# Kernel optimization log

Measured on AMD Instinct MI355X. Metric: run time of the kernel, lower is better.

## Reference

```python
import jax, jax.numpy as jnp
import numpy as np

DIM = 1024
D_STATE = 16
D_CONV = 4
EXPAND = 2
D_INNER = EXPAND * DIM          # 2048
DT_RANK = (DIM + 15) // 16      # 64 (math.ceil(d_model/16))
BSZ = 2
SEQ = 2048


def setup_inputs() -> dict:
    key = jax.random.key(0)
    ks = jax.random.split(key, 8)
    g = lambda k, shape, scale: (jax.random.normal(k, shape, jnp.float32) * scale)
    return {
        "x": g(ks[0], (BSZ, SEQ, DIM), 1.0),
        # in_proj: Linear(d_model -> 2*d_inner, bias=False)
        "W_in": g(ks[1], (2 * D_INNER, DIM), DIM ** -0.5),
        # depthwise causal conv1d: groups=d_inner, kernel d_conv, bias=True
        "conv_w": g(ks[2], (D_INNER, 1, D_CONV), D_CONV ** -0.5),
        "conv_b": jnp.zeros((D_INNER,), jnp.float32),
        # x_proj: Linear(d_inner -> dt_rank + 2*d_state, bias=False)
        "W_xproj": g(ks[3], (DT_RANK + 2 * D_STATE, D_INNER), D_INNER ** -0.5),
        # dt_proj: Linear(dt_rank -> d_inner, bias=True)
        "W_dt": g(ks[4], (D_INNER, DT_RANK), DT_RANK ** -0.5),
        "b_dt": g(ks[5], (D_INNER,), 0.1),
        # S4D-real init: A = -exp(A_log), A_log = log(1..d_state)
        "A_log": jnp.log(jnp.broadcast_to(
            jnp.arange(1, D_STATE + 1, dtype=jnp.float32), (D_INNER, D_STATE))),
        "D": jnp.ones((D_INNER,), jnp.float32),
        # out_proj: Linear(d_inner -> d_model, bias=False)
        "W_out": g(ks[6], (DIM, D_INNER), D_INNER ** -0.5),
        # wrapper LayerNorm(dim)
        "gamma": jnp.ones((DIM,), jnp.float32),
        "beta": jnp.zeros((DIM,), jnp.float32),
    }


def reference(x, W_in, conv_w, conv_b, W_xproj, W_dt, b_dt,
              A_log, D, W_out, gamma, beta):
    B, L, _ = x.shape
    # ---- input projection, split into conv path and gate ----
    xz = x @ W_in.T                              # (B, L, 2*d_inner)
    xc, z = jnp.split(xz, 2, axis=-1)
    # ---- depthwise causal conv1d + SiLU ----
    xt = jnp.transpose(xc, (0, 2, 1))            # (B, d_inner, L)
    conv = jax.lax.conv_general_dilated(
        xt, conv_w, window_strides=(1,), padding=[(D_CONV - 1, 0)],
        dimension_numbers=("NCH", "OIH", "NCH"), feature_group_count=D_INNER)
    u = jax.nn.silu(jnp.transpose(conv + conv_b[None, :, None], (0, 2, 1)))  # (B,L,d_inner)
    # ---- input-dependent delta, B, C ----
    xdbc = u @ W_xproj.T                          # (B, L, dt_rank + 2*d_state)
    dt = xdbc[..., :DT_RANK]
    Bm = xdbc[..., DT_RANK:DT_RANK + D_STATE]     # (B, L, d_state)
    Cm = xdbc[..., DT_RANK + D_STATE:]            # (B, L, d_state)
    delta = jax.nn.softplus(dt @ W_dt.T + b_dt)   # (B, L, d_inner)
    A = -jnp.exp(A_log)                           # (d_inner, d_state)
    # ---- selective scan: h_t = exp(dt*A) h_{t-1} + dt*B_t*u_t ; y_t = <h_t, C_t> ----
    def step(h, inputs):
        d_t, u_t, B_t, C_t = inputs               # (B,d_inner),(B,d_inner),(B,S),(B,S)
        dA = jnp.exp(d_t[:, :, None] * A)         # (B, d_inner, S)
        h = h * dA + (d_t * u_t)[:, :, None] * B_t[:, None, :]
        y = jnp.einsum("bds,bs->bd", h, C_t)
        return h, y
    tm = lambda a: jnp.transpose(a, (1, 0, 2))    # time-major for scan
    h0 = jnp.zeros((B, D_INNER, D_STATE), x.dtype)
    _, ys = jax.lax.scan(step, h0, (tm(delta), tm(u), tm(Bm), tm(Cm)))
    y = jnp.transpose(ys, (1, 0, 2)) + u * D      # skip term D*u
    y = y * jax.nn.silu(z)                        # gate
    out = y @ W_out.T                             # (B, L, dim)
    # ---- wrapper LayerNorm(dim), eps=1e-5 ----
    mean = out.mean(-1, keepdims=True)
    var = out.var(-1, keepdims=True)
    return (out - mean) * jax.lax.rsqrt(var + 1e-5) * gamma + beta
```

## Files before the change

### kernel.cpp

```cpp
#include <hip/hip_runtime.h>
#include <stdint.h>

typedef unsigned short u16;
typedef __bf16 bf16x8 __attribute__((ext_vector_type(8)));
typedef unsigned short u16x8 __attribute__((ext_vector_type(8)));
typedef unsigned short u16x4 __attribute__((ext_vector_type(4)));
typedef float f32x4 __attribute__((ext_vector_type(4)));

#define BSZ 2
#define SEQ 2048
#define DIM 1024
#define D_INNER 2048
#define DT_RANK 64
#define D_STATE 16
#define XPROJ_N 96
#define NCHUNK 32
#define CHUNK_T 64
#define LOG2E 1.44269504f

#define N_X   4194304
#define N_W   4194304
#define N_WX  196608
#define N_WDT 131072
#define N_WO  2097152
#define N_XD  393216

__device__ __forceinline__ float bf2f(u16 h) {
    return __uint_as_float(((unsigned)h) << 16);
}
__device__ __forceinline__ u16 f2bf(float f) {
    unsigned u = __float_as_uint(f);
    unsigned r = (u + 0x7FFFu + ((u >> 16) & 1u)) >> 16;
    return (u16)r;
}

__device__ __forceinline__ f32x4 mfma16(bf16x8 a, bf16x8 b, f32x4 c) {
    return __builtin_amdgcn_mfma_f32_16x16x32_bf16(a, b, c, 0, 0, 0);
}

__device__ __forceinline__ void gload_lds16(const void* g, void* l) {
    __builtin_amdgcn_global_load_lds(
        (const __attribute__((address_space(1))) unsigned int*)(uintptr_t)g,
        (__attribute__((address_space(3))) unsigned int*)(uintptr_t)l,
        16, 0, 0);
}

__device__ __forceinline__ void split4(const float* __restrict__ in,
                                       u16* __restrict__ hi, u16* __restrict__ lo,
                                       long i)
{
    f32x4 v = *(const f32x4*)(in + i);
    u16x4 h, l;
    #pragma unroll
    for (int j = 0; j < 4; j++) {
        u16 hh = f2bf(v[j]);
        h[j] = hh;
        l[j] = f2bf(v[j] - bf2f(hh));
    }
    *(u16x4*)(hi + i) = h;
    *(u16x4*)(lo + i) = l;
}

__global__ __launch_bounds__(256)
void megasplit4(const float* __restrict__ x,  u16* __restrict__ xh,  u16* __restrict__ xl,
                const float* __restrict__ w,  u16* __restrict__ wh,  u16* __restrict__ wl,
                const float* __restrict__ wx, u16* __restrict__ wxh, u16* __restrict__ wxl,
                const float* __restrict__ wd, u16* __restrict__ wdh, u16* __restrict__ wdl)
{
    long i = ((long)blockIdx.x * 256 + threadIdx.x) * 4;
    if (i < N_X) { split4(x, xh, xl, i); return; }
    i -= N_X;
    if (i < N_W) { split4(w, wh, wl, i); return; }
    i -= N_W;
    if (i < N_WX) { split4(wx, wxh, wxl, i); return; }
    i -= N_WX;
    if (i < N_WDT) { split4(wd, wdh, wdl, i); }
}

#define PH_TOP                                                                \
    __builtin_amdgcn_sched_barrier(0);                                        \
    __builtin_amdgcn_s_barrier();                                             \
    asm volatile("s_waitcnt lgkmcnt(0)" ::: "memory");                        \
    __builtin_amdgcn_sched_barrier(0);                                        \
    __builtin_amdgcn_s_setprio(1);
#define PH_BOT                                                                \
    __builtin_amdgcn_s_setprio(0);                                            \
    __builtin_amdgcn_sched_barrier(0);                                        \
    __builtin_amdgcn_s_barrier();

__global__ __launch_bounds__(512, 2)
void gemm256_xz(const u16* __restrict__ xh, const u16* __restrict__ xl,
                const u16* __restrict__ wh, const u16* __restrict__ wl,
                u16* __restrict__ xc, float* __restrict__ z)
{
    __shared__ u16 lds[65536];

    const int tid  = threadIdx.x;
    const int w    = tid >> 6;
    const int lane = tid & 63;
    const int r16  = lane & 15;
    const int quad = lane >> 4;
    const int wr   = w >> 2;
    const int wc   = w & 3;
    const long m0  = (long)blockIdx.y * 256;
    const long n0  = (long)blockIdx.x * 256;

    const int c0 = tid, c1 = tid + 512;
    const int ma0 = c0 >> 2, kc0 = ((c0 & 3) ^ ((ma0 >> 1) & 3)) * 8;
    const int ma1 = c1 >> 2, kc1 = ((c1 & 3) ^ ((ma1 >> 1) & 3)) * 8;
    const int arow0 = ((int)m0 + ma0) * DIM + kc0;
    const int arow1 = ((int)m0 + ma1) * DIM + kc1;
    const int brow0 = ((int)n0 + ma0) * DIM + kc0;
    const int brow1 = ((int)n0 + ma1) * DIM + kc1;

    int caof[8], cbof[4];
    #pragma unroll
    for (int i = 0; i < 8; i++) {
        int m = wr * 128 + i * 16 + r16;
        caof[i] = (m * 4 + (quad ^ ((m >> 1) & 3))) * 8;
    }
    #pragma unroll
    for (int j = 0; j < 4; j++) {
        int n = wc * 64 + j * 16 + r16;
        cbof[j] = (n * 4 + (quad ^ ((n >> 1) & 3))) * 8;
    }

    f32x4 acc[8][4];
    #pragma unroll
    for (int i = 0; i < 8; i++)
        #pragma unroll
        for (int j = 0; j < 4; j++) acc[i][j] = {0.f, 0.f, 0.f, 0.f};

    gload_lds16(xh + arow0, lds + c0 * 8);
    gload_lds16(xh + arow1, lds + c1 * 8);
    gload_lds16(xl + arow0, lds + 8192 + c0 * 8);
    gload_lds16(xl + arow1, lds + 8192 + c1 * 8);
    gload_lds16(wh + brow0, lds + 16384 + c0 * 8);
    gload_lds16(wh + brow1, lds + 16384 + c1 * 8);
    gload_lds16(wl + brow0, lds + 24576 + c0 * 8);
    gload_lds16(wl + brow1, lds + 24576 + c1 * 8);
    asm volatile("s_waitcnt vmcnt(0)" ::: "memory");
    __builtin_amdgcn_s_barrier();

    int kt = 0;
#define XZ_FTILE(CUR, SN)                                                     \
  {                                                                           \
    int st = kt + 1; if (st > 31) st = 31;                                    \
    const int kb = st * 32;                                                   \
    const u16* AHp = lds + (CUR) * 32768;                                     \
    const u16* ALp = AHp + 8192;                                              \
    const u16* BHp = AHp + 16384;                                             \
    const u16* BLp = AHp + 24576;                                             \
    u16* Sb = lds + (SN) * 32768;                                             \
    bf16x8 a0[4], a1[4], fbh[4], fbl[4];                                      \
                            \
    _Pragma("unroll") for (int j = 0; j < 4; j++)                             \
        fbh[j] = *(const bf16x8*)(BHp + cbof[j]);                             \
    _Pragma("unroll") for (int i = 0; i < 4; i++)                             \
        a0[i] = *(const bf16x8*)(AHp + caof[i]);                              \
    gload_lds16(xh + arow0 + kb, Sb + c0 * 8);                                \
    gload_lds16(xh + arow1 + kb, Sb + c1 * 8);                                \
    PH_TOP                                                                    \
    _Pragma("unroll") for (int i = 0; i < 4; i++)                             \
      _Pragma("unroll") for (int j = 0; j < 4; j++)                           \
        acc[i][j] = mfma16(a0[i], fbh[j], acc[i][j]);                         \
    PH_BOT                                                                    \
                                \
    _Pragma("unroll") for (int i = 0; i < 4; i++)                             \
        a1[i] = *(const bf16x8*)(AHp + caof[4 + i]);                          \
    gload_lds16(xl + arow0 + kb, Sb + 8192 + c0 * 8);                         \
    gload_lds16(xl + arow1 + kb, Sb + 8192 + c1 * 8);                         \
    PH_TOP                                                                    \
    _Pragma("unroll") for (int i = 0; i < 4; i++)                             \
      _Pragma("unroll") for (int j = 0; j < 4; j++)                           \
        acc[4 + i][j] = mfma16(a1[i], fbh[j], acc[4 + i][j]);                 \
    PH_BOT                                                                    \
                        \
    _Pragma("unroll") for (int j = 0; j < 4; j++)                             \
        fbl[j] = *(const bf16x8*)(BLp + cbof[j]);                             \
    gload_lds16(wh + brow0 + kb, Sb + 16384 + c0 * 8);                        \
    gload_lds16(wh + brow1 + kb, Sb + 16384 + c1 * 8);                        \
    PH_TOP                                                                    \
    _Pragma("unroll") for (int i = 0; i < 4; i++)                             \
      _Pragma("unroll") for (int j = 0; j < 4; j++)                           \
        acc[i][j] = mfma16(a0[i], fbl[j], acc[i][j]);                         \
    PH_BOT                                                                    \
                             \
    gload_lds16(wl + brow0 + kb, Sb + 24576 + c0 * 8);                        \
    gload_lds16(wl + brow1 + kb, Sb + 24576 + c1 * 8);                        \
    PH_TOP                                                                    \
    _Pragma("unroll") for (int i = 0; i < 4; i++)                             \
      _Pragma("unroll") for (int j = 0; j < 4; j++)                           \
        acc[4 + i][j] = mfma16(a1[i], fbl[j], acc[4 + i][j]);                 \
    PH_BOT                                                                    \
                   \
    _Pragma("unroll") for (int i = 0; i < 4; i++)                             \
        a0[i] = *(const bf16x8*)(ALp + caof[i]);                              \
    PH_TOP                                                                    \
    _Pragma("unroll") for (int i = 0; i < 4; i++)                             \
      _Pragma("unroll") for (int j = 0; j < 4; j++)                           \
        acc[i][j] = mfma16(a0[i], fbh[j], acc[i][j]);                         \
    PH_BOT                                                                    \
                      \
    _Pragma("unroll") for (int i = 0; i < 4; i++)                             \
        a1[i] = *(const bf16x8*)(ALp + caof[4 + i]);                          \
    PH_TOP                                                                    \
    _Pragma("unroll") for (int i = 0; i < 4; i++)                             \
      _Pragma("unroll") for (int j = 0; j < 4; j++)                           \
        acc[4 + i][j] = mfma16(a1[i], fbh[j], acc[4 + i][j]);                 \
    __builtin_amdgcn_s_setprio(0);                                            \
    __builtin_amdgcn_sched_barrier(0);                                        \
    asm volatile("s_waitcnt vmcnt(0)" ::: "memory");                          \
    __builtin_amdgcn_s_barrier();                                             \
    kt++;                                                                     \
  }

    #pragma unroll 1
    for (int it = 0; it < 16; it++) {
        XZ_FTILE(0, 1)
        XZ_FTILE(1, 0)
    }
#undef XZ_FTILE

    asm volatile("s_waitcnt vmcnt(0)" ::: "memory");

    const bool isz = (n0 >= 2048);
    #pragma unroll
    for (int i = 0; i < 8; i++) {
        #pragma unroll
        for (int j = 0; j < 4; j++) {
            long col = n0 + wc * 64 + j * 16 + r16;
            #pragma unroll
            for (int r = 0; r < 4; r++) {
                long row = m0 + wr * 128 + i * 16 + quad * 4 + r;
                if (!isz) xc[row * (long)D_INNER + col] = f2bf(acc[i][j][r]);
                else      z[row * (long)D_INNER + (col - D_INNER)] = acc[i][j][r];
            }
        }
    }
}

__global__ __launch_bounds__(512, 2)
void gemm256_out(const u16* __restrict__ A, const u16* __restrict__ Bh,
                 const u16* __restrict__ Bl, float* __restrict__ OutBase)
{
    __shared__ u16 lds[40960];

    const int tid  = threadIdx.x;
    const int w    = tid >> 6;
    const int lane = tid & 63;
    const int r16  = lane & 15;
    const int quad = lane >> 4;
    const int wr   = w >> 2;
    const int wc   = w & 3;
    const long m0  = (long)blockIdx.y * 128;
    const long n0  = (long)blockIdx.x * 256;
    const int  kz  = blockIdx.z;
    const int  kbase = kz * 1024;
    float* Out = OutBase + (long)kz * 4194304;

    const int maA = tid >> 2, kcA = ((tid & 3) ^ ((maA >> 1) & 3)) * 8;
    const int arow = ((int)m0 + maA) * D_INNER + kbase + kcA;
    const int c0 = tid, c1 = tid + 512;
    const int mb0 = c0 >> 2, kb0 = ((c0 & 3) ^ ((mb0 >> 1) & 3)) * 8;
    const int mb1 = c1 >> 2, kb1 = ((c1 & 3) ^ ((mb1 >> 1) & 3)) * 8;
    const int brow0 = ((int)n0 + mb0) * D_INNER + kbase + kb0;
    const int brow1 = ((int)n0 + mb1) * D_INNER + kbase + kb1;

    int caof[4], cbof[4];
    #pragma unroll
    for (int i = 0; i < 4; i++) {
        int m = wr * 64 + i * 16 + r16;
        caof[i] = (m * 4 + (quad ^ ((m >> 1) & 3))) * 8;
    }
    #pragma unroll
    for (int j = 0; j < 4; j++) {
        int n = wc * 64 + j * 16 + r16;
        cbof[j] = (n * 4 + (quad ^ ((n >> 1) & 3))) * 8;
    }

    f32x4 acc[4][4];
    #pragma unroll
    for (int i = 0; i < 4; i++)
        #pragma unroll
        for (int j = 0; j < 4; j++) acc[i][j] = {0.f, 0.f, 0.f, 0.f};

    gload_lds16(A  + arow,  lds + tid * 8);
    gload_lds16(Bh + brow0, lds + 4096 + c0 * 8);
    gload_lds16(Bh + brow1, lds + 4096 + c1 * 8);
    gload_lds16(Bl + brow0, lds + 12288 + c0 * 8);
    gload_lds16(Bl + brow1, lds + 12288 + c1 * 8);
    asm volatile("s_waitcnt vmcnt(0)" ::: "memory");
    __builtin_amdgcn_s_barrier();

    int kt = 0;
#define O2_TILE(CUR, SN)                                                      \
  {                                                                           \
    int st = kt + 1; if (st > 31) st = 31;                                    \
    const int kb = st * 32;                                                   \
    const u16* Ap  = lds + (CUR) * 20480;                                     \
    const u16* BHp = Ap + 4096;                                               \
    const u16* BLp = Ap + 12288;                                              \
    u16* Sb = lds + (SN) * 20480;                                             \
    bf16x8 fa[4], fb[4];                                                      \
                            \
    _Pragma("unroll") for (int j = 0; j < 4; j++)                             \
        fb[j] = *(const bf16x8*)(BHp + cbof[j]);                              \
    _Pragma("unroll") for (int i = 0; i < 4; i++)                             \
        fa[i] = *(const bf16x8*)(Ap + caof[i]);                               \
    gload_lds16(A + arow + kb, Sb + tid * 8);                                 \
    PH_TOP                                                                    \
    _Pragma("unroll") for (int i = 0; i < 4; i++)                             \
      _Pragma("unroll") for (int j = 0; j < 4; j++)                           \
        acc[i][j] = mfma16(fa[i], fb[j], acc[i][j]);                          \
    PH_BOT                                                                    \
                 \
    _Pragma("unroll") for (int j = 0; j < 4; j++)                             \
        fb[j] = *(const bf16x8*)(BLp + cbof[j]);                              \
    gload_lds16(Bh + brow0 + kb, Sb + 4096 + c0 * 8);                         \
    gload_lds16(Bh + brow1 + kb, Sb + 4096 + c1 * 8);                         \
    gload_lds16(Bl + brow0 + kb, Sb + 12288 + c0 * 8);                        \
    gload_lds16(Bl + brow1 + kb, Sb + 12288 + c1 * 8);                        \
    PH_TOP                                                                    \
    _Pragma("unroll") for (int i = 0; i < 4; i++)                             \
      _Pragma("unroll") for (int j = 0; j < 4; j++)                           \
        acc[i][j] = mfma16(fa[i], fb[j], acc[i][j]);                          \
    __builtin_amdgcn_s_setprio(0);                                            \
    __builtin_amdgcn_sched_barrier(0);                                        \
    asm volatile("s_waitcnt vmcnt(0)" ::: "memory");                          \
    __builtin_amdgcn_s_barrier();                                             \
    kt++;                                                                     \
  }

    #pragma unroll 1
    for (int it = 0; it < 16; it++) {
        O2_TILE(0, 1)
        O2_TILE(1, 0)
    }
#undef O2_TILE

    asm volatile("s_waitcnt vmcnt(0)" ::: "memory");

    #pragma unroll
    for (int i = 0; i < 4; i++) {
        #pragma unroll
        for (int j = 0; j < 4; j++) {
            long col = n0 + wc * 64 + j * 16 + r16;
            #pragma unroll
            for (int r = 0; r < 4; r++) {
                long row = m0 + wr * 64 + i * 16 + quad * 4 + r;
                Out[row * (long)DIM + col] = acc[i][j][r];
            }
        }
    }
}

__global__ __launch_bounds__(64)
void gemm_dt32(const u16* __restrict__ Ah, const u16* __restrict__ Al, int lda,
               const u16* __restrict__ Bh, const u16* __restrict__ Bl, int ldb,
               float* __restrict__ C, int ldc, const float* __restrict__ bias)
{
    const int lane = threadIdx.x;
    const int r16  = lane & 15;
    const int quad = lane >> 4;
    const long m0 = (long)blockIdx.y * 32;
    const long n0 = (long)blockIdx.x * 32;

    const u16* Ah0 = Ah + (m0 + r16) * (long)lda + quad * 8;
    const u16* Ah1 = Ah0 + 16L * lda;
    const u16* Al0 = Al + (m0 + r16) * (long)lda + quad * 8;
    const u16* Al1 = Al0 + 16L * lda;
    const u16* Bh0 = Bh + (n0 + r16) * (long)ldb + quad * 8;
    const u16* Bh1 = Bh0 + 16L * ldb;
    const u16* Bl0 = Bl + (n0 + r16) * (long)ldb + quad * 8;
    const u16* Bl1 = Bl0 + 16L * ldb;

    f32x4 acc00 = {0,0,0,0}, acc01 = {0,0,0,0}, acc10 = {0,0,0,0}, acc11 = {0,0,0,0};

    #pragma unroll
    for (int k = 0; k < DT_RANK; k += 32) {
        bf16x8 a0h = *(const bf16x8*)(Ah0 + k);
        bf16x8 a1h = *(const bf16x8*)(Ah1 + k);
        bf16x8 a0l = *(const bf16x8*)(Al0 + k);
        bf16x8 a1l = *(const bf16x8*)(Al1 + k);
        bf16x8 b0h = *(const bf16x8*)(Bh0 + k);
        bf16x8 b1h = *(const bf16x8*)(Bh1 + k);
        bf16x8 b0l = *(const bf16x8*)(Bl0 + k);
        bf16x8 b1l = *(const bf16x8*)(Bl1 + k);
        acc00 = mfma16(a0h, b0h, acc00); acc00 = mfma16(a0h, b0l, acc00); acc00 = mfma16(a0l, b0h, acc00);
        acc01 = mfma16(a0h, b1h, acc01); acc01 = mfma16(a0h, b1l, acc01); acc01 = mfma16(a0l, b1h, acc01);
        acc10 = mfma16(a1h, b0h, acc10); acc10 = mfma16(a1h, b0l, acc10); acc10 = mfma16(a1l, b0h, acc10);
        acc11 = mfma16(a1h, b1h, acc11); acc11 = mfma16(a1h, b1l, acc11); acc11 = mfma16(a1l, b1h, acc11);
    }

    #pragma unroll
    for (int i = 0; i < 2; i++) {
        #pragma unroll
        for (int j = 0; j < 2; j++) {
            f32x4 v = (i == 0) ? (j == 0 ? acc00 : acc01) : (j == 0 ? acc10 : acc11);
            long col = n0 + j * 16 + r16;
            #pragma unroll
            for (int r = 0; r < 4; r++) {
                long row = m0 + i * 16 + quad * 4 + r;
                float x = v[r] + bias[col];
                x = (x > 15.f) ? x : log1pf(__expf(x));
                C[row * (long)ldc + col] = x;
            }
        }
    }
}

__global__ __launch_bounds__(64)
void gemm3_skp(const u16* __restrict__ A, int lda,
               const u16* __restrict__ Bh, const u16* __restrict__ Bl, int ldb,
               float* __restrict__ Cpart, int ldc, int K0)
{
    const int lane = threadIdx.x;
    const int r16  = lane & 15;
    const int quad = lane >> 4;
    const long m0 = (long)blockIdx.y * 32;
    const long n0 = (long)blockIdx.x * 32;
    const int kbase = blockIdx.z * K0;
    float* C = Cpart + (long)blockIdx.z * N_XD;

    const u16* Ap0 = A  + (m0 + r16) * (long)lda + quad * 8 + kbase;
    const u16* Ap1 = Ap0 + 16L * lda;
    const u16* Bh0 = Bh + (n0 + r16) * (long)ldb + quad * 8 + kbase;
    const u16* Bh1 = Bh0 + 16L * ldb;
    const u16* Bl0 = Bl + (n0 + r16) * (long)ldb + quad * 8 + kbase;
    const u16* Bl1 = Bl0 + 16L * ldb;

    f32x4 acc00 = {0,0,0,0}, acc01 = {0,0,0,0}, acc10 = {0,0,0,0}, acc11 = {0,0,0,0};

    for (int k = 0; k < K0; k += 32) {
        bf16x8 a0 = *(const bf16x8*)(Ap0 + k);
        bf16x8 a1 = *(const bf16x8*)(Ap1 + k);
        bf16x8 b0h = *(const bf16x8*)(Bh0 + k);
        bf16x8 b1h = *(const bf16x8*)(Bh1 + k);
        bf16x8 b0l = *(const bf16x8*)(Bl0 + k);
        bf16x8 b1l = *(const bf16x8*)(Bl1 + k);
        acc00 = mfma16(a0, b0h, acc00); acc00 = mfma16(a0, b0l, acc00);
        acc01 = mfma16(a0, b1h, acc01); acc01 = mfma16(a0, b1l, acc01);
        acc10 = mfma16(a1, b0h, acc10); acc10 = mfma16(a1, b0l, acc10);
        acc11 = mfma16(a1, b1h, acc11); acc11 = mfma16(a1, b1l, acc11);
    }

    #pragma unroll
    for (int i = 0; i < 2; i++) {
        #pragma unroll
        for (int j = 0; j < 2; j++) {
            f32x4 v = (i == 0) ? (j == 0 ? acc00 : acc01) : (j == 0 ? acc10 : acc11);
            long col = n0 + j * 16 + r16;
            #pragma unroll
            for (int r = 0; r < 4; r++) {
                long row = m0 + i * 16 + quad * 4 + r;
                C[row * (long)ldc + col] = v[r];
            }
        }
    }
}

__global__ __launch_bounds__(256)
void combine3(const float* __restrict__ part, float* __restrict__ xdbc,
              u16* __restrict__ hi, u16* __restrict__ lo)
{
    long i = ((long)blockIdx.x * 256 + threadIdx.x) * 4;
    if (i >= N_XD) return;
    f32x4 s = *(const f32x4*)(part + i);
    #pragma unroll
    for (int j = 1; j < 8; j++) {
        f32x4 p = *(const f32x4*)(part + (long)j * N_XD + i);
        s[0] += p[0]; s[1] += p[1]; s[2] += p[2]; s[3] += p[3];
    }
    *(f32x4*)(xdbc + i) = s;
    u16x4 h, l;
    #pragma unroll
    for (int j = 0; j < 4; j++) {
        u16 hh = f2bf(s[j]);
        h[j] = hh;
        l[j] = f2bf(s[j] - bf2f(hh));
    }
    *(u16x4*)(hi + i) = h;
    *(u16x4*)(lo + i) = l;
}

__global__ __launch_bounds__(256)
void conv_silu(const u16* __restrict__ xc, const float* __restrict__ cw,
               const float* __restrict__ cb, u16* __restrict__ u)
{
    long idx = ((long)blockIdx.x * 256 + threadIdx.x) * 8;
    int t  = (int)((idx >> 11) & 2047);
    int d0 = (int)(idx & 2047);

    bf16x8 xrow[4];
    #pragma unroll
    for (int j = 0; j < 4; j++) {
        int tt = t - 3 + j;
        if (tt >= 0) xrow[j] = *(const bf16x8*)(xc + idx + (long)(j - 3) * D_INNER);
        else         xrow[j] = bf16x8{0,0,0,0,0,0,0,0};
    }
    u16x8 out;
    #pragma unroll
    for (int e = 0; e < 8; e++) {
        int d = d0 + e;
        float acc = cb[d];
        #pragma unroll
        for (int j = 0; j < 4; j++)
            acc += cw[d * 4 + j] * (float)xrow[j][e];
        out[e] = f2bf(acc / (1.f + __expf(-acc)));
    }
    *(u16x8*)(u + idx) = out;
}

__global__ __launch_bounds__(256)
void scan_partA(const float* __restrict__ delta, const u16* __restrict__ u,
                const float* __restrict__ xdbc, const float* __restrict__ A_log,
                float* __restrict__ hbuf, float* __restrict__ sdelta,
                const float* __restrict__ wout, u16* __restrict__ wouth,
                u16* __restrict__ woutl)
{
    const int d = blockIdx.x * 256 + threadIdx.x;
    const int c = blockIdx.y;
    const int b = blockIdx.z;
    const int t0 = c * CHUNK_T;

    float Af[16];
    #pragma unroll
    for (int s = 0; s < 16; s++) Af[s] = -__expf(A_log[d * 16 + s]) * LOG2E;
    bool fast = true;
    #pragma unroll
    for (int s = 0; s < 16; s++)
        fast = fast && (fabsf(Af[s] - (float)(s + 1) * Af[0]) < 1e-3f * (float)(s + 1));

    float h[16];
    #pragma unroll
    for (int s = 0; s < 16; s++) h[s] = 0.f;
    float sd = 0.f;

    const float* dptr = delta + ((long)b * SEQ + t0) * D_INNER + d;
    const u16*   uptr = u     + ((long)b * SEQ + t0) * D_INNER + d;
    const float* xp   = xdbc  + ((long)b * SEQ + t0) * XPROJ_N;

    if (fast) {
        const float Af0 = Af[0];
        for (int t = 0; t < CHUNK_T; t++) {
            float dl = dptr[(long)t * D_INNER];
            float uu = bf2f(uptr[(long)t * D_INNER]);
            f32x4 B0 = *(const f32x4*)(xp + t * XPROJ_N + DT_RANK);
            f32x4 B1 = *(const f32x4*)(xp + t * XPROJ_N + DT_RANK + 4);
            f32x4 B2 = *(const f32x4*)(xp + t * XPROJ_N + DT_RANK + 8);
            f32x4 B3 = *(const f32x4*)(xp + t * XPROJ_N + DT_RANK + 12);
            float Bv[16] = {B0[0],B0[1],B0[2],B0[3], B1[0],B1[1],B1[2],B1[3],
                            B2[0],B2[1],B2[2],B2[3], B3[0],B3[1],B3[2],B3[3]};
            sd += dl;
            float dlu = dl * uu;
            float q = exp2f(dl * Af0);
            float dAc = 1.f;
            #pragma unroll
            for (int s = 0; s < 16; s++) {
                dAc *= q;
                h[s] = h[s] * dAc + dlu * Bv[s];
            }
        }
    } else {
        for (int t = 0; t < CHUNK_T; t++) {
            float dl = dptr[(long)t * D_INNER];
            float uu = bf2f(uptr[(long)t * D_INNER]);
            f32x4 B0 = *(const f32x4*)(xp + t * XPROJ_N + DT_RANK);
            f32x4 B1 = *(const f32x4*)(xp + t * XPROJ_N + DT_RANK + 4);
            f32x4 B2 = *(const f32x4*)(xp + t * XPROJ_N + DT_RANK + 8);
            f32x4 B3 = *(const f32x4*)(xp + t * XPROJ_N + DT_RANK + 12);
            float Bv[16] = {B0[0],B0[1],B0[2],B0[3], B1[0],B1[1],B1[2],B1[3],
                            B2[0],B2[1],B2[2],B2[3], B3[0],B3[1],B3[2],B3[3]};
            sd += dl;
            float dlu = dl * uu;
            #pragma unroll
            for (int s = 0; s < 16; s++)
                h[s] = h[s] * exp2f(dl * Af[s]) + dlu * Bv[s];
        }
    }

    float* hout = hbuf + ((long)(b * NCHUNK + c) * D_INNER + d) * 16;
    #pragma unroll
    for (int s = 0; s < 16; s++) hout[s] = h[s];
    sdelta[(long)(b * NCHUNK + c) * D_INNER + d] = sd;

    long tidg = (((long)b * NCHUNK + c) * 8 + blockIdx.x) * 256 + threadIdx.x;
    long base = tidg * 16;
    #pragma unroll
    for (int k = 0; k < 4; k++) split4(wout, wouth, woutl, base + 4 * k);
}

__global__ __launch_bounds__(256)
void scan_fixup(float* __restrict__ hbuf, const float* __restrict__ sdelta,
                const float* __restrict__ A_log)
{
    const int idx = blockIdx.x * 256 + threadIdx.x;
    const int ds = idx & (D_INNER * 16 - 1);
    const int b  = idx >> 15;
    const float Af = -__expf(A_log[ds]) * LOG2E;
    float hin = 0.f;
    #pragma unroll 4
    for (int c = 0; c < NCHUNK; c++) {
        long gi = (long)(b * NCHUNK + c) * (D_INNER * 16) + ds;
        float e = hbuf[gi];
        hbuf[gi] = hin;
        float sd = sdelta[(long)(b * NCHUNK + c) * D_INNER + (ds >> 4)];
        hin = e + exp2f(Af * sd) * hin;
    }
}

__global__ __launch_bounds__(256)
void scan_partC(const float* __restrict__ delta, const u16* __restrict__ u,
                const float* __restrict__ xdbc, const float* __restrict__ z,
                const float* __restrict__ A_log, const float* __restrict__ Dp,
                const float* __restrict__ hbuf, u16* __restrict__ y)
{
    const int d = blockIdx.x * 256 + threadIdx.x;
    const int c = blockIdx.y;
    const int b = blockIdx.z;
    const int t0 = c * CHUNK_T;

    float Af[16];
    #pragma unroll
    for (int s = 0; s < 16; s++) Af[s] = -__expf(A_log[d * 16 + s]) * LOG2E;
    bool fast = true;
    #pragma unroll
    for (int s = 0; s < 16; s++)
        fast = fast && (fabsf(Af[s] - (float)(s + 1) * Af[0]) < 1e-3f * (float)(s + 1));
    const float Dd = Dp[d];

    float h[16];
    const float* hin = hbuf + ((long)(b * NCHUNK + c) * D_INNER + d) * 16;
    #pragma unroll
    for (int s = 0; s < 16; s++) h[s] = hin[s];

    const float* dptr = delta + ((long)b * SEQ + t0) * D_INNER + d;
    const u16*   uptr = u     + ((long)b * SEQ + t0) * D_INNER + d;
    const float* zptr = z     + ((long)b * SEQ + t0) * D_INNER + d;
    const float* xp   = xdbc  + ((long)b * SEQ + t0) * XPROJ_N;
    u16* yptr = y + ((long)b * SEQ + t0) * D_INNER + d;

    if (fast) {
        const float Af0 = Af[0];
        for (int t = 0; t < CHUNK_T; t++) {
            float dl = dptr[(long)t * D_INNER];
            float uu = bf2f(uptr[(long)t * D_INNER]);
            float zl = zptr[(long)t * D_INNER];
            f32x4 B0 = *(const f32x4*)(xp + t * XPROJ_N + DT_RANK);
            f32x4 B1 = *(const f32x4*)(xp + t * XPROJ_N + DT_RANK + 4);
            f32x4 B2 = *(const f32x4*)(xp + t * XPROJ_N + DT_RANK + 8);
            f32x4 B3 = *(const f32x4*)(xp + t * XPROJ_N + DT_RANK + 12);
            f32x4 C0 = *(const f32x4*)(xp + t * XPROJ_N + DT_RANK + 16);
            f32x4 C1 = *(const f32x4*)(xp + t * XPROJ_N + DT_RANK + 20);
            f32x4 C2 = *(const f32x4*)(xp + t * XPROJ_N + DT_RANK + 24);
            f32x4 C3 = *(const f32x4*)(xp + t * XPROJ_N + DT_RANK + 28);
            float Bv[16] = {B0[0],B0[1],B0[2],B0[3], B1[0],B1[1],B1[2],B1[3],
                            B2[0],B2[1],B2[2],B2[3], B3[0],B3[1],B3[2],B3[3]};
            float Cv[16] = {C0[0],C0[1],C0[2],C0[3], C1[0],C1[1],C1[2],C1[3],
                            C2[0],C2[1],C2[2],C2[3], C3[0],C3[1],C3[2],C3[3]};
            float dlu = dl * uu;
            float q = exp2f(dl * Af0);
            float dAc = 1.f;
            float p0 = 0.f, p1 = 0.f, p2 = 0.f, p3 = 0.f;
            #pragma unroll
            for (int s = 0; s < 16; s += 4) {
                float dA0 = dAc * q;
                float dA1 = dA0 * q;
                float dA2 = dA1 * q;
                float dA3 = dA2 * q;
                dAc = dA3;
                h[s]   = h[s]   * dA0 + dlu * Bv[s];
                h[s+1] = h[s+1] * dA1 + dlu * Bv[s+1];
                h[s+2] = h[s+2] * dA2 + dlu * Bv[s+2];
                h[s+3] = h[s+3] * dA3 + dlu * Bv[s+3];
                p0 += h[s]   * Cv[s];
                p1 += h[s+1] * Cv[s+1];
                p2 += h[s+2] * Cv[s+2];
                p3 += h[s+3] * Cv[s+3];
            }
            float acc = (p0 + p1) + (p2 + p3);
            float sz = zl / (1.f + __expf(-zl));
            float yy = (acc + uu * Dd) * sz;
            yptr[(long)t * D_INNER] = f2bf(yy);
        }
    } else {
        for (int t = 0; t < CHUNK_T; t++) {
            float dl = dptr[(long)t * D_INNER];
            float uu = bf2f(uptr[(long)t * D_INNER]);
            float zl = zptr[(long)t * D_INNER];
            f32x4 B0 = *(const f32x4*)(xp + t * XPROJ_N + DT_RANK);
            f32x4 B1 = *(const f32x4*)(xp + t * XPROJ_N + DT_RANK + 4);
            f32x4 B2 = *(const f32x4*)(xp + t * XPROJ_N + DT_RANK + 8);
            f32x4 B3 = *(const f32x4*)(xp + t * XPROJ_N + DT_RANK + 12);
            f32x4 C0 = *(const f32x4*)(xp + t * XPROJ_N + DT_RANK + 16);
            f32x4 C1 = *(const f32x4*)(xp + t * XPROJ_N + DT_RANK + 20);
            f32x4 C2 = *(const f32x4*)(xp + t * XPROJ_N + DT_RANK + 24);
            f32x4 C3 = *(const f32x4*)(xp + t * XPROJ_N + DT_RANK + 28);
            float Bv[16] = {B0[0],B0[1],B0[2],B0[3], B1[0],B1[1],B1[2],B1[3],
                            B2[0],B2[1],B2[2],B2[3], B3[0],B3[1],B3[2],B3[3]};
            float Cv[16] = {C0[0],C0[1],C0[2],C0[3], C1[0],C1[1],C1[2],C1[3],
                            C2[0],C2[1],C2[2],C2[3], C3[0],C3[1],C3[2],C3[3]};
            float dlu = dl * uu;
            float p0 = 0.f, p1 = 0.f, p2 = 0.f, p3 = 0.f;
            #pragma unroll
            for (int s = 0; s < 16; s += 4) {
                h[s]   = h[s]   * exp2f(dl * Af[s])   + dlu * Bv[s];
                h[s+1] = h[s+1] * exp2f(dl * Af[s+1]) + dlu * Bv[s+1];
                h[s+2] = h[s+2] * exp2f(dl * Af[s+2]) + dlu * Bv[s+2];
                h[s+3] = h[s+3] * exp2f(dl * Af[s+3]) + dlu * Bv[s+3];
                p0 += h[s]   * Cv[s];
                p1 += h[s+1] * Cv[s+1];
                p2 += h[s+2] * Cv[s+2];
                p3 += h[s+3] * Cv[s+3];
            }
            float acc = (p0 + p1) + (p2 + p3);
            float sz = zl / (1.f + __expf(-zl));
            float yy = (acc + uu * Dd) * sz;
            yptr[(long)t * D_INNER] = f2bf(yy);
        }
    }
}

__global__ __launch_bounds__(256)
void layernorm_kernel(const float* __restrict__ p0,
                      const float* __restrict__ gamma, const float* __restrict__ beta,
                      float* __restrict__ out)
{
    const long row = blockIdx.x;
    const long base = row * DIM;
    int tid = threadIdx.x;
    float v[4];
    float sum = 0.f, sq = 0.f;
    #pragma unroll
    for (int i = 0; i < 4; i++) {
        long c = base + tid + i * 256;
        v[i] = p0[c] + p0[c + 4194304];
        sum += v[i];
        sq  += v[i] * v[i];
    }
    #pragma unroll
    for (int off = 1; off < 64; off <<= 1) {
        sum += __shfl_xor(sum, off);
        sq  += __shfl_xor(sq, off);
    }
    __shared__ float ssum[4], ssq[4];
    int w = tid >> 6;
    if ((tid & 63) == 0) { ssum[w] = sum; ssq[w] = sq; }
    __syncthreads();
    float ts = ssum[0] + ssum[1] + ssum[2] + ssum[3];
    float tq = ssq[0] + ssq[1] + ssq[2] + ssq[3];
    float mean = ts * (1.f / DIM);
    float var  = tq * (1.f / DIM) - mean * mean;
    float rstd = rsqrtf(var + 1e-5f);
    float* o = out + base;
    #pragma unroll
    for (int i = 0; i < 4; i++) {
        int c = tid + i * 256;
        o[c] = (v[i] - mean) * rstd * gamma[c] + beta[c];
    }
}

extern "C" void kernel_launch(void* const* d_in, const int* in_sizes, int n_in,
                              void* d_out, int out_size, void* d_ws, size_t ws_size,
                              hipStream_t stream)
{
    const float* x      = (const float*)d_in[0];
    const float* W_in   = (const float*)d_in[1];
    const float* conv_w = (const float*)d_in[2];
    const float* conv_b = (const float*)d_in[3];
    const float* W_xproj= (const float*)d_in[4];
    const float* W_dt   = (const float*)d_in[5];
    const float* b_dt   = (const float*)d_in[6];
    const float* A_log  = (const float*)d_in[7];
    const float* Dv     = (const float*)d_in[8];
    const float* W_out  = (const float*)d_in[9];
    const float* gamma  = (const float*)d_in[10];
    const float* beta   = (const float*)d_in[11];

    char* ws = (char*)d_ws;
    u16*   xc    = (u16*)(ws);
    float* g3p   = (float*)(ws);
    u16*   xdh   = (u16*)(ws + 12582912);
    u16*   xdl   = (u16*)(ws + 14155776);
    float* hbuf  = (float*)(ws);
    u16*   wouth = (u16*)(ws + 8388608);
    u16*   woutl = (u16*)(ws + 12582912);
    float* z     = (float*)(ws + 16777216);
    float* opre  = (float*)(ws + 16777216);
    u16*   u     = (u16*)(ws + 50331648);
    u16*   xh    = (u16*)(ws + 67108864);
    u16*   xl    = (u16*)(ws + 75497472);
    u16*   wh    = (u16*)(ws + 83886080);
    u16*   wl    = (u16*)(ws + 92274688);
    float* delta = (float*)(ws + 67108864);
    float* xdbc  = (float*)(ws + 100663296);
    u16*   wxh   = (u16*)(ws + 102236160);
    u16*   wxl   = (u16*)(ws + 102629376);
    u16*   wdth  = (u16*)(ws + 103022592);
    u16*   wdtl  = (u16*)(ws + 103284736);
    float* sdel  = (float*)(ws + 103546880);
    u16*   yb    = (u16*)d_out;

    megasplit4<<<8512, 256, 0, stream>>>(x, xh, xl, W_in, wh, wl,
                                         W_xproj, wxh, wxl, W_dt, wdth, wdtl);
    gemm256_xz<<<dim3(16, 16), 512, 0, stream>>>(xh, xl, wh, wl, xc, z);
    conv_silu<<<4096, 256, 0, stream>>>(xc, conv_w, conv_b, u);
    gemm3_skp<<<dim3(3, 128, 8), 64, 0, stream>>>(
        u, D_INNER, wxh, wxl, D_INNER, g3p, XPROJ_N, 256);
    combine3<<<384, 256, 0, stream>>>(g3p, xdbc, xdh, xdl);
    gemm_dt32<<<dim3(64, 128), 64, 0, stream>>>(
        xdh, xdl, XPROJ_N, wdth, wdtl, DT_RANK, delta, D_INNER, b_dt);
    scan_partA<<<dim3(8, NCHUNK, BSZ), 256, 0, stream>>>(
        delta, u, xdbc, A_log, hbuf, sdel, W_out, wouth, woutl);
    scan_fixup<<<256, 256, 0, stream>>>(hbuf, sdel, A_log);
    scan_partC<<<dim3(8, NCHUNK, BSZ), 256, 0, stream>>>(delta, u, xdbc, z, A_log, Dv, hbuf, yb);
    gemm256_out<<<dim3(4, 32, 2), 512, 0, stream>>>(yb, wouth, woutl, opre);
    layernorm_kernel<<<4096, 256, 0, stream>>>(opre, gamma, beta, (float*)d_out);
}
```

Measured before the change: 385.9 us.

## Shrink xz GEMM tile to 128x128 and prefetch scan fixup loads

The in_proj GEMM moves from 256x256 tiles with 512 threads to 128x128 tiles with 256 threads, which quadruples the grid from 256 to 1024 blocks and halves LDS use per block. The aim is better occupancy and load balance across the CUs. The cost is lower data reuse per block and more global traffic for the operands. Separately, scan_fixup now loads the next chunk's hbuf and sdelta values one iteration early, so those loads overlap the serial recurrence.

```diff
diff --git a/kernel.cpp b/kernel.cpp
--- a/kernel.cpp
+++ b/kernel.cpp
@@ -88,24 +88,24 @@
     __builtin_amdgcn_sched_barrier(0);                                        \
     __builtin_amdgcn_s_barrier();
 
-__global__ __launch_bounds__(512, 2)
+__global__ __launch_bounds__(256, 2)
 void gemm256_xz(const u16* __restrict__ xh, const u16* __restrict__ xl,
                 const u16* __restrict__ wh, const u16* __restrict__ wl,
                 u16* __restrict__ xc, float* __restrict__ z)
 {
-    __shared__ u16 lds[65536];
+    __shared__ u16 lds[32768];
 
     const int tid  = threadIdx.x;
     const int w    = tid >> 6;
     const int lane = tid & 63;
     const int r16  = lane & 15;
     const int quad = lane >> 4;
-    const int wr   = w >> 2;
-    const int wc   = w & 3;
-    const long m0  = (long)blockIdx.y * 256;
-    const long n0  = (long)blockIdx.x * 256;
-
-    const int c0 = tid, c1 = tid + 512;
+    const int wr   = w >> 1;
+    const int wc   = w & 1;
+    const long m0  = (long)blockIdx.y * 128;
+    const long n0  = (long)blockIdx.x * 128;
+
+    const int c0 = tid, c1 = tid + 256;
     const int ma0 = c0 >> 2, kc0 = ((c0 & 3) ^ ((ma0 >> 1) & 3)) * 8;
     const int ma1 = c1 >> 2, kc1 = ((c1 & 3) ^ ((ma1 >> 1) & 3)) * 8;
     const int arow0 = ((int)m0 + ma0) * DIM + kc0;
@@ -113,10 +113,10 @@
     const int brow0 = ((int)n0 + ma0) * DIM + kc0;
     const int brow1 = ((int)n0 + ma1) * DIM + kc1;
 
-    int caof[8], cbof[4];
-    #pragma unroll
-    for (int i = 0; i < 8; i++) {
-        int m = wr * 128 + i * 16 + r16;
+    int caof[4], cbof[4];
+    #pragma unroll
+    for (int i = 0; i < 4; i++) {
+        int m = wr * 64 + i * 16 + r16;
         caof[i] = (m * 4 + (quad ^ ((m >> 1) & 3))) * 8;
     }
     #pragma unroll
@@ -125,20 +125,20 @@
         cbof[j] = (n * 4 + (quad ^ ((n >> 1) & 3))) * 8;
     }
 
-    f32x4 acc[8][4];
-    #pragma unroll
-    for (int i = 0; i < 8; i++)
+    f32x4 acc[4][4];
+    #pragma unroll
+    for (int i = 0; i < 4; i++)
         #pragma unroll
         for (int j = 0; j < 4; j++) acc[i][j] = {0.f, 0.f, 0.f, 0.f};
 
     gload_lds16(xh + arow0, lds + c0 * 8);
     gload_lds16(xh + arow1, lds + c1 * 8);
-    gload_lds16(xl + arow0, lds + 8192 + c0 * 8);
-    gload_lds16(xl + arow1, lds + 8192 + c1 * 8);
-    gload_lds16(wh + brow0, lds + 16384 + c0 * 8);
-    gload_lds16(wh + brow1, lds + 16384 + c1 * 8);
-    gload_lds16(wl + brow0, lds + 24576 + c0 * 8);
-    gload_lds16(wl + brow1, lds + 24576 + c1 * 8);
+    gload_lds16(xl + arow0, lds + 4096 + c0 * 8);
+    gload_lds16(xl + arow1, lds + 4096 + c1 * 8);
+    gload_lds16(wh + brow0, lds + 8192 + c0 * 8);
+    gload_lds16(wh + brow1, lds + 8192 + c1 * 8);
+    gload_lds16(wl + brow0, lds + 12288 + c0 * 8);
+    gload_lds16(wl + brow1, lds + 12288 + c1 * 8);
     asm volatile("s_waitcnt vmcnt(0)" ::: "memory");
     __builtin_amdgcn_s_barrier();
 
@@ -147,67 +147,45 @@
   {                                                                           \
     int st = kt + 1; if (st > 31) st = 31;                                    \
     const int kb = st * 32;                                                   \
-    const u16* AHp = lds + (CUR) * 32768;                                     \
-    const u16* ALp = AHp + 8192;                                              \
-    const u16* BHp = AHp + 16384;                                             \
-    const u16* BLp = AHp + 24576;                                             \
-    u16* Sb = lds + (SN) * 32768;                                             \
-    bf16x8 a0[4], a1[4], fbh[4], fbl[4];                                      \
-                            \
+    const u16* AHp = lds + (CUR) * 16384;                                     \
+    const u16* ALp = AHp + 4096;                                              \
+    const u16* BHp = AHp + 8192;                                              \
+    const u16* BLp = AHp + 12288;                                             \
+    u16* Sb = lds + (SN) * 16384;                                             \
+    bf16x8 fa[4], fbh[4], fbl[4];                                             \
+                        \
     _Pragma("unroll") for (int j = 0; j < 4; j++)                             \
         fbh[j] = *(const bf16x8*)(BHp + cbof[j]);                             \
     _Pragma("unroll") for (int i = 0; i < 4; i++)                             \
-        a0[i] = *(const bf16x8*)(AHp + caof[i]);                              \
+        fa[i] = *(const bf16x8*)(AHp + caof[i]);                              \
     gload_lds16(xh + arow0 + kb, Sb + c0 * 8);                                \
     gload_lds16(xh + arow1 + kb, Sb + c1 * 8);                                \
+    gload_lds16(xl + arow0 + kb, Sb + 4096 + c0 * 8);                         \
+    gload_lds16(xl + arow1 + kb, Sb + 4096 + c1 * 8);                         \
     PH_TOP                                                                    \
     _Pragma("unroll") for (int i = 0; i < 4; i++)                             \
       _Pragma("unroll") for (int j = 0; j < 4; j++)                           \
-        acc[i][j] = mfma16(a0[i], fbh[j], acc[i][j]);                         \
+        acc[i][j] = mfma16(fa[i], fbh[j], acc[i][j]);                         \
     PH_BOT                                                                    \
-                                \
-    _Pragma("unroll") for (int i = 0; i < 4; i++)                             \
-        a1[i] = *(const bf16x8*)(AHp + caof[4 + i]);                          \
-    gload_lds16(xl + arow0 + kb, Sb + 8192 + c0 * 8);                         \
-    gload_lds16(xl + arow1 + kb, Sb + 8192 + c1 * 8);                         \
+                            \
+    _Pragma("unroll") for (int j = 0; j < 4; j++)                             \
+        fbl[j] = *(const bf16x8*)(BLp + cbof[j]);                             \
+    gload_lds16(wh + brow0 + kb, Sb + 8192 + c0 * 8);                         \
+    gload_lds16(wh + brow1 + kb, Sb + 8192 + c1 * 8);                         \
+    gload_lds16(wl + brow0 + kb, Sb + 12288 + c0 * 8);                        \
+    gload_lds16(wl + brow1 + kb, Sb + 12288 + c1 * 8);                        \
     PH_TOP                                                                    \
     _Pragma("unroll") for (int i = 0; i < 4; i++)                             \
       _Pragma("unroll") for (int j = 0; j < 4; j++)                           \
-        acc[4 + i][j] = mfma16(a1[i], fbh[j], acc[4 + i][j]);                 \
+        acc[i][j] = mfma16(fa[i], fbl[j], acc[i][j]);                         \
     PH_BOT                                                                    \
-                        \
-    _Pragma("unroll") for (int j = 0; j < 4; j++)                             \
-        fbl[j] = *(const bf16x8*)(BLp + cbof[j]);                             \
-    gload_lds16(wh + brow0 + kb, Sb + 16384 + c0 * 8);                        \
-    gload_lds16(wh + brow1 + kb, Sb + 16384 + c1 * 8);                        \
+          \
+    _Pragma("unroll") for (int i = 0; i < 4; i++)                             \
+        fa[i] = *(const bf16x8*)(ALp + caof[i]);                              \
     PH_TOP                                                                    \
     _Pragma("unroll") for (int i = 0; i < 4; i++)                             \
       _Pragma("unroll") for (int j = 0; j < 4; j++)                           \
-        acc[i][j] = mfma16(a0[i], fbl[j], acc[i][j]);                         \
-    PH_BOT                                                                    \
-                             \
-    gload_lds16(wl + brow0 + kb, Sb + 24576 + c0 * 8);                        \
-    gload_lds16(wl + brow1 + kb, Sb + 24576 + c1 * 8);                        \
-    PH_TOP                                                                    \
-    _Pragma("unroll") for (int i = 0; i < 4; i++)                             \
-      _Pragma("unroll") for (int j = 0; j < 4; j++)                           \
-        acc[4 + i][j] = mfma16(a1[i], fbl[j], acc[4 + i][j]);                 \
-    PH_BOT                                                                    \
-                   \
-    _Pragma("unroll") for (int i = 0; i < 4; i++)                             \
-        a0[i] = *(const bf16x8*)(ALp + caof[i]);                              \
-    PH_TOP                                                                    \
-    _Pragma("unroll") for (int i = 0; i < 4; i++)                             \
-      _Pragma("unroll") for (int j = 0; j < 4; j++)                           \
-        acc[i][j] = mfma16(a0[i], fbh[j], acc[i][j]);                         \
-    PH_BOT                                                                    \
-                      \
-    _Pragma("unroll") for (int i = 0; i < 4; i++)                             \
-        a1[i] = *(const bf16x8*)(ALp + caof[4 + i]);                          \
-    PH_TOP                                                                    \
-    _Pragma("unroll") for (int i = 0; i < 4; i++)                             \
-      _Pragma("unroll") for (int j = 0; j < 4; j++)                           \
-        acc[4 + i][j] = mfma16(a1[i], fbh[j], acc[4 + i][j]);                 \
+        acc[i][j] = mfma16(fa[i], fbh[j], acc[i][j]);                         \
     __builtin_amdgcn_s_setprio(0);                                            \
     __builtin_amdgcn_sched_barrier(0);                                        \
     asm volatile("s_waitcnt vmcnt(0)" ::: "memory");                          \
@@ -226,13 +204,13 @@
 
     const bool isz = (n0 >= 2048);
     #pragma unroll
-    for (int i = 0; i < 8; i++) {
+    for (int i = 0; i < 4; i++) {
         #pragma unroll
         for (int j = 0; j < 4; j++) {
             long col = n0 + wc * 64 + j * 16 + r16;
             #pragma unroll
             for (int r = 0; r < 4; r++) {
-                long row = m0 + wr * 128 + i * 16 + quad * 4 + r;
+                long row = m0 + wr * 64 + i * 16 + quad * 4 + r;
                 if (!isz) xc[row * (long)D_INNER + col] = f2bf(acc[i][j][r]);
                 else      z[row * (long)D_INNER + (col - D_INNER)] = acc[i][j][r];
             }
@@ -600,13 +578,20 @@
     const int b  = idx >> 15;
     const float Af = -__expf(A_log[ds]) * LOG2E;
     float hin = 0.f;
+    long gi = (long)b * NCHUNK * (D_INNER * 16) + ds;
+    long si = (long)b * NCHUNK * D_INNER + (ds >> 4);
+    float e  = hbuf[gi];
+    float sd = sdelta[si];
     #pragma unroll 4
     for (int c = 0; c < NCHUNK; c++) {
-        long gi = (long)(b * NCHUNK + c) * (D_INNER * 16) + ds;
-        float e = hbuf[gi];
+        int cn = (c + 1 < NCHUNK) ? (c + 1) : (NCHUNK - 1);
+        long gin = (long)(b * NCHUNK + cn) * (D_INNER * 16) + ds;
+        long sin = (long)(b * NCHUNK + cn) * D_INNER + (ds >> 4);
+        float e2  = hbuf[gin];
+        float sd2 = sdelta[sin];
         hbuf[gi] = hin;
-        float sd = sdelta[(long)(b * NCHUNK + c) * D_INNER + (ds >> 4)];
         hin = e + exp2f(Af * sd) * hin;
+        e = e2; sd = sd2; gi = gin;
     }
 }
 
@@ -804,7 +789,7 @@
 
     megasplit4<<<8512, 256, 0, stream>>>(x, xh, xl, W_in, wh, wl,
                                          W_xproj, wxh, wxl, W_dt, wdth, wdtl);
-    gemm256_xz<<<dim3(16, 16), 512, 0, stream>>>(xh, xl, wh, wl, xc, z);
+    gemm256_xz<<<dim3(32, 32), 256, 0, stream>>>(xh, xl, wh, wl, xc, z);
     conv_silu<<<4096, 256, 0, stream>>>(xc, conv_w, conv_b, u);
     gemm3_skp<<<dim3(3, 128, 8), 64, 0, stream>>>(
         u, D_INNER, wxh, wxl, D_INNER, g3p, XPROJ_N, 256);
```

Result: slower. 402.4 us (+4.3%).
